# Kernel tuning notes

Measured on AMD Instinct MI355X. Metric: run time of the kernel, lower is better.

The kernel has to match this reference:

```python
import jax, jax.numpy as jnp
import numpy as np

# Fixed architecture constants from AlgelogicNetwork.__init__
M, J, I, L, W = 4, 2, 3, 2, 9
B = 1048576  # batch size (only free dim)


def setup_inputs() -> dict:
    key = jax.random.key(0)
    ks = jax.random.split(key, 7)
    state = jax.random.normal(ks[0], (B, W * L), dtype=jnp.float32)
    # rule.constants ~ U(-1, 1), rule.gammas ~ U(0, 1), stacked over M rules
    constants = jax.random.uniform(ks[1], (M, J, L), minval=-1.0, maxval=1.0, dtype=jnp.float32)
    gammas = jax.random.uniform(ks[2], (M, J, L), dtype=jnp.float32)
    # body Linears (L -> I), one per (rule m, premise j); head Linear (I -> L) per rule
    W_body = jax.random.normal(ks[3], (M, J, I, L), dtype=jnp.float32) * 0.5
    b_body = jax.random.normal(ks[4], (M, J, I), dtype=jnp.float32) * 0.1
    W_head = jax.random.normal(ks[5], (M, L, I), dtype=jnp.float32) * 0.5
    b_head = jax.random.normal(ks[6], (M, L), dtype=jnp.float32) * 0.1
    return {
        "state": state,
        "constants": constants,
        "gammas": gammas,
        "W_body": W_body,
        "b_body": b_body,
        "W_head": W_head,
        "b_head": b_head,
    }


def reference(state, constants, gammas, W_body, b_body, W_head, b_head):
    s = state.reshape(-1, W, L)                       # [B, W, L]
    g = jnp.clip(gammas, 0.0, 1.0)                    # sigmoid() in source = clamp; [M, J, L]
    wgt = 1.0 - g                                     # [M, J, L]

    # match_scores[m,j,b,w] = sum_l (1-g[m,j,l]) * (const[m,j,l] - s[b,w,l])^2
    # L=2 fixed: unroll over l to avoid a [M,J,B,W,L] intermediate
    ms = sum(
        wgt[:, :, l, None, None]
        * (constants[:, :, l, None, None] - s[None, None, :, :, l]) ** 2
        for l in range(L)
    )                                                  # [M, J, B, W]

    attn = jax.nn.softmax(-ms, axis=-1)                # softmax over W positions (temperature=1)
    best = jnp.einsum('mjbw,bwl->mjbl', attn, s)       # soft-gathered propositions
    match_quality = jnp.sum(attn * ms, axis=-1).sum(axis=1)   # [M, B], summed over premises j

    captured = jnp.einsum('mjbl,mjil->mjbi', best, W_body) + b_body[:, :, None, :]  # body Linear
    g_avg = g.mean(axis=-1)                            # [M, J]
    captured_vars = jnp.einsum('mj,mjbi->mbi', g_avg, captured)                     # [M, B, I]

    rule_out = jnp.einsum('mbi,mli->mbl', captured_vars, W_head) + b_head[:, None, :]  # [M, B, L]

    # similarity[m,b,w] = -sum_l (rule_out[m,b,l] - s[b,w,l])^2
    sim = -jnp.sum((rule_out[:, :, None, :] - s[None]) ** 2, axis=-1)  # [M, B, W]
    confidence = jnp.exp(-match_quality)               # [M, B]
    return jnp.einsum('mb,mbw->bw', confidence, sim)   # [B, W]
```

## Files before the change

kernel.cpp:

```cpp
#include <hip/hip_runtime.h>

namespace {
constexpr int kM = 4, kJ = 2, kI = 3, kL = 2, kW = 9;
constexpr float kInvLn2 = 1.4426950408889634f;

typedef float v2f __attribute__((ext_vector_type(2)));

__device__ __forceinline__ float fexp2(float x) { return __builtin_amdgcn_exp2f(x); }

__global__ void prep_kernel(const float* __restrict__ constants,
                            const float* __restrict__ gammas,
                            const float* __restrict__ W_body,
                            const float* __restrict__ b_body,
                            const float* __restrict__ W_head,
                            const float* __restrict__ b_head,
                            float* __restrict__ dp) {
  const int t = threadIdx.x;
  if (t < 8) {
    const int mj = t, m = t >> 1, j = t & 1;
    const float g0 = fminf(fmaxf(gammas[mj * kL + 0], 0.f), 1.f);
    const float g1 = fminf(fmaxf(gammas[mj * kL + 1], 0.f), 1.f);
    const float w0 = 1.f - g0, w1 = 1.f - g1;
    const float c0 = constants[mj * kL + 0], c1 = constants[mj * kL + 1];
    const float gavg = 0.5f * (g0 + g1);
    float* base = dp + m * 18;
    base[0 * 2 + j] = (w0 * c0 * c0 + w1 * c1 * c1) * kInvLn2;
    base[1 * 2 + j] = -2.f * w0 * c0 * kInvLn2;
    base[2 * 2 + j] = -2.f * w1 * c1 * kInvLn2;
    base[3 * 2 + j] = w0 * kInvLn2;
    base[4 * 2 + j] = w1 * kInvLn2;
    for (int l = 0; l < kL; ++l)
      for (int lp = 0; lp < kL; ++lp) {
        float acc = 0.f;
        for (int i = 0; i < kI; ++i)
          acc += W_head[(m * kL + l) * kI + i] * W_body[(mj * kI + i) * kL + lp];
        base[(5 + l * kL + lp) * 2 + j] = gavg * acc;
      }
  } else if (t < 12) {
    const int m = t - 8;
    for (int l = 0; l < kL; ++l) {
      float d = b_head[m * kL + l];
      for (int j = 0; j < kJ; ++j) {
        const int mj = m * kJ + j;
        const float g0 = fminf(fmaxf(gammas[mj * kL + 0], 0.f), 1.f);
        const float g1 = fminf(fmaxf(gammas[mj * kL + 1], 0.f), 1.f);
        const float gavg = 0.5f * (g0 + g1);
        float acc = 0.f;
        for (int i = 0; i < kI; ++i)
          acc += W_head[(m * kL + l) * kI + i] * b_body[mj * kI + i];
        d += gavg * acc;
      }
      dp[72 + m * kL + l] = d;
    }
  }
}

__global__ __launch_bounds__(128, 6) void algelogic_main(
    const float* __restrict__ state, const float* __restrict__ dp,
    float* __restrict__ out) {
  __shared__ float sdp[80];
  const int t = threadIdx.x;

  if (t < 80) sdp[t] = dp[t];

  const int b = blockIdx.x * 128 + t;
  const float* srow = state + (size_t)b * (kW * kL);
  v2f sv[kW];
#pragma unroll
  for (int w = 0; w < kW; ++w) {
    const float2 v = *reinterpret_cast<const float2*>(srow + 2 * w);
    v2f s; s.x = v.x; s.y = v.y;
    sv[w] = s;
  }
  __syncthreads();

  float Cs = 0.f, X0 = 0.f, X1 = 0.f, K = 0.f;
#pragma unroll
  for (int m = 0; m < kM; ++m) {
    const v2f* pp = reinterpret_cast<const v2f*>(sdp + m * 18);
    const v2f A = pp[0], B0 = pp[1], B1 = pp[2], w0 = pp[3], w1 = pp[4];

    v2f msP[kW];
    v2f mn = {3.4e38f, 3.4e38f};
#pragma unroll
    for (int w = 0; w < kW; ++w) {
      const float s0w = sv[w].x, s1w = sv[w].y;
      const v2f t0 = B0 + w0 * s0w;
      const v2f t1 = B1 + w1 * s1w;
      v2f v = A + t0 * s0w;
      v += t1 * s1w;
      msP[w] = v;
      mn = __builtin_elementwise_min(mn, v);
    }

    v2f psum = {0.f, 0.f}, pb0 = {0.f, 0.f}, pb1 = {0.f, 0.f}, pmq = {0.f, 0.f};
#pragma unroll
    for (int w = 0; w < kW; ++w) {
      const v2f d = mn - msP[w];
      v2f e; e.x = fexp2(d.x); e.y = fexp2(d.y);
      psum += e;
      pb0 += e * sv[w].x;
      pb1 += e * sv[w].y;
      pmq += e * msP[w];
    }

    v2f rinv;
    rinv.x = __builtin_amdgcn_rcpf(psum.x);
    rinv.y = __builtin_amdgcn_rcpf(psum.y);
    const v2f bb0 = pb0 * rinv, bb1 = pb1 * rinv;
    const v2f mqP = pmq * rinv;
    const float mq2 = mqP.x + mqP.y;
    const float conf = fexp2(-mq2);

    const v2f C00 = pp[5], C01 = pp[6], C10 = pp[7], C11 = pp[8];
    const v2f t0 = C00 * bb0 + C01 * bb1;
    const v2f t1 = C10 * bb0 + C11 * bb1;
    const float r0 = sdp[72 + m * 2 + 0] + t0.x + t0.y;
    const float r1 = sdp[72 + m * 2 + 1] + t1.x + t1.y;

    Cs += conf;
    X0 = fmaf(conf, r0, X0);
    X1 = fmaf(conf, r1, X1);
    K = fmaf(conf, fmaf(r0, r0, r1 * r1), K);
  }

  const float X02 = 2.f * X0, X12 = 2.f * X1;
  float* orow = out + (size_t)b * kW;
#pragma unroll
  for (int w = 0; w < kW; ++w) {
    const v2f q = sv[w] * sv[w];
    const float qs = q.x + q.y;
    orow[w] = fmaf(X02, sv[w].x, fmaf(X12, sv[w].y, fmaf(-Cs, qs, -K)));
  }
}
}

extern "C" void kernel_launch(void* const* d_in, const int* in_sizes, int n_in,
                              void* d_out, int out_size, void* d_ws, size_t ws_size,
                              hipStream_t stream) {
  const float* state     = (const float*)d_in[0];
  const float* constants = (const float*)d_in[1];
  const float* gammas    = (const float*)d_in[2];
  const float* W_body    = (const float*)d_in[3];
  const float* b_body    = (const float*)d_in[4];
  const float* W_head    = (const float*)d_in[5];
  const float* b_head    = (const float*)d_in[6];
  float* out = (float*)d_out;
  float* dp  = (float*)d_ws;

  const int B = in_sizes[0] / (kW * kL);
  hipLaunchKernelGGL(prep_kernel, dim3(1), dim3(64), 0, stream,
                     constants, gammas, W_body, b_body, W_head, b_head, dp);
  hipLaunchKernelGGL(algelogic_main, dim3(B / 128), dim3(128), 0, stream,
                     state, dp, out);
}
```

Baseline: 35.99 us.

## Process two batch rows per thread with float4 loads and drop softmax max pass

```diff
diff --git a/kernel.cpp b/kernel.cpp
--- a/kernel.cpp
+++ b/kernel.cpp
@@ -24,11 +24,11 @@
     const float c0 = constants[mj * kL + 0], c1 = constants[mj * kL + 1];
     const float gavg = 0.5f * (g0 + g1);
     float* base = dp + m * 18;
-    base[0 * 2 + j] = (w0 * c0 * c0 + w1 * c1 * c1) * kInvLn2;
-    base[1 * 2 + j] = -2.f * w0 * c0 * kInvLn2;
-    base[2 * 2 + j] = -2.f * w1 * c1 * kInvLn2;
-    base[3 * 2 + j] = w0 * kInvLn2;
-    base[4 * 2 + j] = w1 * kInvLn2;
+    base[0 * 2 + j] = -(w0 * c0 * c0 + w1 * c1 * c1) * kInvLn2;
+    base[1 * 2 + j] = 2.f * w0 * c0 * kInvLn2;
+    base[2 * 2 + j] = 2.f * w1 * c1 * kInvLn2;
+    base[3 * 2 + j] = -w0 * kInvLn2;
+    base[4 * 2 + j] = -w1 * kInvLn2;
     for (int l = 0; l < kL; ++l)
       for (int lp = 0; lp < kL; ++lp) {
         float acc = 0.f;
@@ -55,82 +55,95 @@
   }
 }
 
-__global__ __launch_bounds__(128, 6) void algelogic_main(
+__global__ __launch_bounds__(256) void algelogic_main(
     const float* __restrict__ state, const float* __restrict__ dp,
     float* __restrict__ out) {
-  __shared__ float sdp[80];
-  const int t = threadIdx.x;
+  const int p = blockIdx.x * 256 + threadIdx.x;
+  const float4* sq = reinterpret_cast<const float4*>(state) + (size_t)p * 9;
 
-  if (t < 80) sdp[t] = dp[t];
+  float4 sF[9];
+#pragma unroll
+  for (int k = 0; k < 9; ++k) sF[k] = sq[k];
 
-  const int b = blockIdx.x * 128 + t;
-  const float* srow = state + (size_t)b * (kW * kL);
-  v2f sv[kW];
-#pragma unroll
-  for (int w = 0; w < kW; ++w) {
-    const float2 v = *reinterpret_cast<const float2*>(srow + 2 * w);
-    v2f s; s.x = v.x; s.y = v.y;
-    sv[w] = s;
-  }
-  __syncthreads();
+  auto sv = [&](int elem, int w) -> v2f {
+    const int g = elem * 9 + w;
+    const float4 f = sF[g >> 1];
+    v2f r;
+    if (g & 1) { r.x = f.z; r.y = f.w; } else { r.x = f.x; r.y = f.y; }
+    return r;
+  };
 
-  float Cs = 0.f, X0 = 0.f, X1 = 0.f, K = 0.f;
+  float Cs[2] = {0.f, 0.f}, X0[2] = {0.f, 0.f}, X1[2] = {0.f, 0.f}, K[2] = {0.f, 0.f};
+
 #pragma unroll
   for (int m = 0; m < kM; ++m) {
-    const v2f* pp = reinterpret_cast<const v2f*>(sdp + m * 18);
-    const v2f A = pp[0], B0 = pp[1], B1 = pp[2], w0 = pp[3], w1 = pp[4];
+    const float* P = dp + m * 18;
+    v2f A, B0, B1, w0, w1, C00, C01, C10, C11;
+    A.x = P[0]; A.y = P[1];  B0.x = P[2]; B0.y = P[3];
+    B1.x = P[4]; B1.y = P[5]; w0.x = P[6]; w0.y = P[7];
+    w1.x = P[8]; w1.y = P[9]; C00.x = P[10]; C00.y = P[11];
+    C01.x = P[12]; C01.y = P[13]; C10.x = P[14]; C10.y = P[15];
+    C11.x = P[16]; C11.y = P[17];
+    const float D0 = dp[72 + m * 2 + 0], D1 = dp[72 + m * 2 + 1];
 
-    v2f msP[kW];
-    v2f mn = {3.4e38f, 3.4e38f};
 #pragma unroll
-    for (int w = 0; w < kW; ++w) {
-      const float s0w = sv[w].x, s1w = sv[w].y;
-      const v2f t0 = B0 + w0 * s0w;
-      const v2f t1 = B1 + w1 * s1w;
-      v2f v = A + t0 * s0w;
-      v += t1 * s1w;
-      msP[w] = v;
-      mn = __builtin_elementwise_min(mn, v);
+    for (int elem = 0; elem < 2; ++elem) {
+      v2f psum = {1e-35f, 1e-35f};
+      v2f pb0 = {0.f, 0.f}, pb1 = {0.f, 0.f}, pmq = {0.f, 0.f};
+#pragma unroll
+      for (int w = 0; w < kW; ++w) {
+        const v2f s = sv(elem, w);
+        const v2f t0 = B0 + w0 * s.x;
+        const v2f t1 = B1 + w1 * s.y;
+        v2f msN = A + t0 * s.x;
+        msN += t1 * s.y;
+        v2f e; e.x = fexp2(msN.x); e.y = fexp2(msN.y);
+        psum += e;
+        pb0 += e * s.x;
+        pb1 += e * s.y;
+        pmq += e * msN;
+      }
+      v2f rinv;
+      rinv.x = __builtin_amdgcn_rcpf(psum.x);
+      rinv.y = __builtin_amdgcn_rcpf(psum.y);
+      const v2f bb0 = pb0 * rinv, bb1 = pb1 * rinv;
+      const v2f mqv = pmq * rinv;
+      const float conf = fexp2(mqv.x + mqv.y);
+
+      const v2f t0 = C00 * bb0 + C01 * bb1;
+      const v2f t1 = C10 * bb0 + C11 * bb1;
+      const float r0 = D0 + t0.x + t0.y;
+      const float r1 = D1 + t1.x + t1.y;
+
+      Cs[elem] += conf;
+      X0[elem] = fmaf(conf, r0, X0[elem]);
+      X1[elem] = fmaf(conf, r1, X1[elem]);
+      K[elem] = fmaf(conf, fmaf(r0, r0, r1 * r1), K[elem]);
     }
-
-    v2f psum = {0.f, 0.f}, pb0 = {0.f, 0.f}, pb1 = {0.f, 0.f}, pmq = {0.f, 0.f};
-#pragma unroll
-    for (int w = 0; w < kW; ++w) {
-      const v2f d = mn - msP[w];
-      v2f e; e.x = fexp2(d.x); e.y = fexp2(d.y);
-      psum += e;
-      pb0 += e * sv[w].x;
-      pb1 += e * sv[w].y;
-      pmq += e * msP[w];
-    }
-
-    v2f rinv;
-    rinv.x = __builtin_amdgcn_rcpf(psum.x);
-    rinv.y = __builtin_amdgcn_rcpf(psum.y);
-    const v2f bb0 = pb0 * rinv, bb1 = pb1 * rinv;
-    const v2f mqP = pmq * rinv;
-    const float mq2 = mqP.x + mqP.y;
-    const float conf = fexp2(-mq2);
-
-    const v2f C00 = pp[5], C01 = pp[6], C10 = pp[7], C11 = pp[8];
-    const v2f t0 = C00 * bb0 + C01 * bb1;
-    const v2f t1 = C10 * bb0 + C11 * bb1;
-    const float r0 = sdp[72 + m * 2 + 0] + t0.x + t0.y;
-    const float r1 = sdp[72 + m * 2 + 1] + t1.x + t1.y;
-
-    Cs += conf;
-    X0 = fmaf(conf, r0, X0);
-    X1 = fmaf(conf, r1, X1);
-    K = fmaf(conf, fmaf(r0, r0, r1 * r1), K);
   }
 
-  const float X02 = 2.f * X0, X12 = 2.f * X1;
-  float* orow = out + (size_t)b * kW;
+  float* orow = out + (size_t)p * (2 * kW);
 #pragma unroll
-  for (int w = 0; w < kW; ++w) {
-    const v2f q = sv[w] * sv[w];
-    const float qs = q.x + q.y;
-    orow[w] = fmaf(X02, sv[w].x, fmaf(X12, sv[w].y, fmaf(-Cs, qs, -K)));
+  for (int elem = 0; elem < 2; ++elem) {
+    const float X02 = 2.f * X0[elem], X12 = 2.f * X1[elem];
+    const float Csl = Cs[elem], Kl = K[elem];
+#pragma unroll
+    for (int w = 0; w < kW; w += 2) {
+      float2 o;
+      {
+        const v2f s = sv(elem, w);
+        const v2f q = s * s;
+        o.x = fmaf(X02, s.x, fmaf(X12, s.y, fmaf(-Csl, q.x + q.y, -Kl)));
+      }
+      if (w + 1 < kW) {
+        const v2f s = sv(elem, w + 1);
+        const v2f q = s * s;
+        o.y = fmaf(X02, s.x, fmaf(X12, s.y, fmaf(-Csl, q.x + q.y, -Kl)));
+        *reinterpret_cast<float2*>(orow + elem * kW + w) = o;
+      } else {
+        orow[elem * kW + w] = o.x;
+      }
+    }
   }
 }
 }
@@ -149,8 +162,9 @@
   float* dp  = (float*)d_ws;
 
   const int B = in_sizes[0] / (kW * kL);
+  const int pairs = B / 2;
   hipLaunchKernelGGL(prep_kernel, dim3(1), dim3(64), 0, stream,
                      constants, gammas, W_body, b_body, W_head, b_head, dp);
-  hipLaunchKernelGGL(algelogic_main, dim3(B / 128), dim3(128), 0, stream,
+  hipLaunchKernelGGL(algelogic_main, dim3(pairs / 256), dim3(256), 0, stream,
                      state, dp, out);
 }
```

Result: slower. 40.53 us (+12.6%).
